# Kernel optimization log

Measured on AMD Instinct MI355X. Metric: run time of the kernel, lower is better.

Reference implementation:

```python
import jax, jax.numpy as jnp
import numpy as np

N = 50000      # nodes
E = 800000     # edges
H = 4          # heads (all layers)
D = 64         # per-head out dim (n_hidden == n_classes == 64)
IN = 256       # in_feats; also H*D so identity residual is valid
NEG_SLOPE = 0.2


def setup_inputs() -> dict:
    key = jax.random.key(0)
    ks = jax.random.split(key, 16)
    x = jax.random.normal(ks[0], (N, IN), dtype=jnp.float32)
    src = jax.random.randint(ks[1], (E,), 0, N, dtype=jnp.int32)
    dst = jax.random.randint(ks[2], (E,), 0, N, dtype=jnp.int32)
    inp = {"x": x, "src": src, "dst": dst}
    fan_ins = [IN, H * D, H * D]  # layer input widths
    for i, fin in enumerate(fan_ins):
        s = 1.0 / np.sqrt(fin)
        inp[f"W{i}"] = jax.random.normal(ks[3 + 4 * i], (fin, H * D), dtype=jnp.float32) * s
        inp[f"al{i}"] = jax.random.normal(ks[4 + 4 * i], (H, D), dtype=jnp.float32) * s
        inp[f"ar{i}"] = jax.random.normal(ks[5 + 4 * i], (H, D), dtype=jnp.float32) * s
        inp[f"b{i}"] = jnp.zeros((H * D,), dtype=jnp.float32)
    return inp


def _gat_layer(h, src, dst, W, al, ar, b, residual, activate):
    # project: [N, in] @ [in, H*D] -> [N, H, D]
    feat = (h @ W).reshape(-1, H, D)
    el = jnp.sum(feat * al, axis=-1)            # [N, H]
    er = jnp.sum(feat * ar, axis=-1)            # [N, H]
    e = jax.nn.leaky_relu(el[src] + er[dst], NEG_SLOPE)  # [E, H]
    # edge softmax per destination node (stable: subtract per-dst max)
    emax = jax.ops.segment_max(e, dst, num_segments=N)  # [N, H]
    e = jnp.exp(e - emax[dst])
    denom = jax.ops.segment_sum(e, dst, num_segments=N)  # [N, H]
    alpha = e / denom[dst]                               # [E, H]
    # message + scatter-aggregate: [E, H, D] summed into [N, H, D]
    out = jax.ops.segment_sum(alpha[:, :, None] * feat[src], dst, num_segments=N)
    if residual:
        out = out + h.reshape(-1, H, D)  # identity residual (in == H*D)
    out = out + b.reshape(1, H, D)
    if activate:
        out = jax.nn.elu(out)
    return out


def reference(x, src, dst, W0, al0, ar0, b0, W1, al1, ar1, b1, W2, al2, ar2, b2):
    h = _gat_layer(x, src, dst, W0, al0, ar0, b0, False, True).reshape(N, H * D)
    h = _gat_layer(h, src, dst, W1, al1, ar1, b1, True, True).reshape(N, H * D)
    h = _gat_layer(h, src, dst, W2, al2, ar2, b2, True, False).mean(axis=1)  # [N, D]
    return h
```

## Files before the change

### kernel.cpp

```cpp
#include <hip/hip_runtime.h>
#include <math.h>

#define N_NODES 50000
#define N_EDGES 800000
#define HD 256
#define NHEAD 4
#define DH 64

typedef short bf16x8 __attribute__((ext_vector_type(8)));
typedef float f32x4 __attribute__((ext_vector_type(4)));

__device__ __forceinline__ unsigned short f2bf(float f) {
    unsigned u = __float_as_uint(f);
    return (unsigned short)((u + 0x7fffu + ((u >> 16) & 1u)) >> 16);
}
__device__ __forceinline__ float bf2f(unsigned short h) {
    return __uint_as_float((unsigned)h << 16);
}

__global__ void packw_k(const float* __restrict__ W0, const float* __restrict__ W1,
                        const float* __restrict__ W2, unsigned short* __restrict__ Wp) {
    int blk = blockIdx.x;
    int L = blk >> 7, t = blk & 127;
    const float* W = L == 0 ? W0 : L == 1 ? W1 : W2;
    int nt = t >> 3, kt = t & 7;
    int lane = threadIdx.x;
    int col = nt * 16 + (lane & 15);
    int kb = kt * 32 + (lane >> 4) * 8;
    unsigned short v[8];
#pragma unroll
    for (int j = 0; j < 8; j++) v[j] = f2bf(W[(size_t)(kb + j) * 256 + col]);
    *(bf16x8*)(Wp + ((size_t)(L * 128 + t) * 64 + lane) * 8) = *(bf16x8*)v;
}

template <bool AFP32>
__global__ __launch_bounds__(256) void gemm_k(const void* __restrict__ Av,
                                              const unsigned short* __restrict__ Wp,
                                              const float* __restrict__ al,
                                              const float* __restrict__ ar,
                                              unsigned short* __restrict__ C,
                                              float* __restrict__ el,
                                              float* __restrict__ er, int M) {
    __shared__ unsigned short Asl[64 * 256];
    int tid = threadIdx.x, wv = tid >> 6, lane = tid & 63;
    int bm = blockIdx.x * 64;
    if (AFP32) {
        const float* A = (const float*)Av;
#pragma unroll
        for (int i = 0; i < 8; i++) {
            int chunk = i * 256 + tid;
            int r = chunk >> 5, kc = (chunk & 31) * 8;
            float4 f0, f1;
            if (bm + r < M) {
                const float* p = A + (size_t)(bm + r) * 256 + kc;
                f0 = *(const float4*)p;
                f1 = *(const float4*)(p + 4);
            } else {
                f0 = f1 = make_float4(0.f, 0.f, 0.f, 0.f);
            }
            unsigned short tmp[8] = {f2bf(f0.x), f2bf(f0.y), f2bf(f0.z), f2bf(f0.w),
                                     f2bf(f1.x), f2bf(f1.y), f2bf(f1.z), f2bf(f1.w)};
            int b = (r * 512 + kc * 2) ^ ((r & 7) << 4);
            *(bf16x8*)((char*)Asl + b) = *(bf16x8*)tmp;
        }
    } else {
        const unsigned short* A = (const unsigned short*)Av;
#pragma unroll
        for (int i = 0; i < 8; i++) {
            int chunk = i * 256 + tid;
            int r = chunk >> 5, c16 = chunk & 31;
            int grow = bm + r; if (grow >= M) grow = M - 1;
            bf16x8 v = *(const bf16x8*)(A + (size_t)grow * 256 + c16 * 8);
            int b = (r * 512 + c16 * 16) ^ ((r & 7) << 4);
            *(bf16x8*)((char*)Asl + b) = v;
        }
    }
    __syncthreads();
    f32x4 acc[4][4] = {};
    const unsigned short* wbase = Wp + (size_t)(wv * 4) * 8 * 64 * 8;
#pragma unroll
    for (int kk = 0; kk < 8; kk++) {
        bf16x8 a[4], b[4];
#pragma unroll
        for (int m = 0; m < 4; m++) {
            int r = m * 16 + (lane & 15);
            int kb = kk * 32 + (lane >> 4) * 8;
            int byt = (r * 512 + kb * 2) ^ ((r & 7) << 4);
            a[m] = *(const bf16x8*)((const char*)Asl + byt);
        }
#pragma unroll
        for (int n = 0; n < 4; n++)
            b[n] = *(const bf16x8*)(wbase + ((size_t)(n * 8 + kk) * 64 + lane) * 8);
#pragma unroll
        for (int m = 0; m < 4; m++)
#pragma unroll
            for (int n = 0; n < 4; n++)
                acc[m][n] = __builtin_amdgcn_mfma_f32_16x16x32_bf16(a[m], b[n],
                                                                    acc[m][n], 0, 0, 0);
    }
    int rr = lane >> 4, cc = lane & 15;
    float alv[4], arv[4];
#pragma unroll
    for (int n = 0; n < 4; n++) {
        alv[n] = al[wv * 64 + n * 16 + cc];
        arv[n] = ar[wv * 64 + n * 16 + cc];
    }
#pragma unroll
    for (int m = 0; m < 4; m++) {
#pragma unroll
        for (int r = 0; r < 4; r++) {
            int row = bm + m * 16 + rr * 4 + r;
            float ep = 0.f, rp = 0.f;
#pragma unroll
            for (int n = 0; n < 4; n++) {
                ep = fmaf(acc[m][n][r], alv[n], ep);
                rp = fmaf(acc[m][n][r], arv[n], rp);
            }
#pragma unroll
            for (int o = 1; o < 16; o <<= 1) {
                ep += __shfl_xor(ep, o);
                rp += __shfl_xor(rp, o);
            }
            if (row < M) {
                if (cc == 0) {
                    el[(size_t)row * NHEAD + wv] = ep;
                    er[(size_t)row * NHEAD + wv] = rp;
                }
#pragma unroll
                for (int n = 0; n < 4; n++)
                    C[(size_t)row * 256 + wv * 64 + n * 16 + cc] = f2bf(acc[m][n][r]);
            }
        }
    }
}

__global__ void hist_k(const int* __restrict__ dst, int* __restrict__ deg) {
    int e = blockIdx.x * 256 + threadIdx.x;
    if (e < N_EDGES) atomicAdd(&deg[dst[e]], 1);
}

__global__ __launch_bounds__(1024) void scan1_k(const int* __restrict__ deg,
                                                int* __restrict__ rowptr,
                                                int* __restrict__ bsum) {
    __shared__ int wsum[16];
    int tid = threadIdx.x, lane = tid & 63, wv = tid >> 6;
    int i = blockIdx.x * 1024 + tid;
    int v = (i < N_NODES) ? deg[i] : 0;
    int sc = v;
#pragma unroll
    for (int o = 1; o < 64; o <<= 1) {
        int t = __shfl_up(sc, o);
        if (lane >= o) sc += t;
    }
    if (lane == 63) wsum[wv] = sc;
    __syncthreads();
    if (wv == 0 && lane < 16) {
        int ws = wsum[lane];
#pragma unroll
        for (int o = 1; o < 16; o <<= 1) {
            int t = __shfl_up(ws, o);
            if (lane >= o) ws += t;
        }
        wsum[lane] = ws;
    }
    __syncthreads();
    int incl = sc + (wv > 0 ? wsum[wv - 1] : 0);
    if (i < N_NODES) rowptr[i + 1] = incl;
    if (tid == 1023) bsum[blockIdx.x] = incl;
}

__global__ __launch_bounds__(1024) void scan3_k(int* __restrict__ rowptr,
                                                const int* __restrict__ bsum,
                                                int* __restrict__ cursor, int nb) {
    __shared__ int boff_s;
    int tid = threadIdx.x;
    if (tid < 64) {
        int v = (tid < nb) ? bsum[tid] : 0;
        int sc = v;
#pragma unroll
        for (int o = 1; o < 64; o <<= 1) {
            int t = __shfl_up(sc, o);
            if ((tid & 63) >= o) sc += t;
        }
        if (tid == (int)blockIdx.x) boff_s = sc - v;
    }
    __syncthreads();
    int off = boff_s;
    int i = blockIdx.x * 1024 + tid;
    if (blockIdx.x == 0 && tid == 0) { rowptr[0] = 0; cursor[0] = 0; }
    if (i < N_NODES) {
        int v = rowptr[i + 1] + off;
        rowptr[i + 1] = v;
        if (i + 1 < N_NODES) cursor[i + 1] = v;
    }
}

__global__ void scatter_k(const int* __restrict__ src, const int* __restrict__ dst,
                          int* __restrict__ cursor, int* __restrict__ csr_src) {
    int e = blockIdx.x * 256 + threadIdx.x;
    if (e >= N_EDGES) return;
    int pos = atomicAdd(&cursor[dst[e]], 1);
    csr_src[pos] = src[e];
}

template <int MODE>
__global__ __launch_bounds__(256) void agg_k(const int* __restrict__ rowptr,
                                             const int* __restrict__ csr_src,
                                             const float* __restrict__ el,
                                             const float* __restrict__ er,
                                             const unsigned short* __restrict__ feat,
                                             const unsigned short* __restrict__ resid,
                                             const float* __restrict__ bias,
                                             float* __restrict__ out,
                                             unsigned short* __restrict__ hb) {
    __shared__ int   ws_s[4][64];
    __shared__ float ws_w[4][4][68];
    int wv = threadIdx.x >> 6, lane = threadIdx.x & 63;
    int node = blockIdx.x * 4 + wv;
    if (node >= N_NODES) return;
    int beg = rowptr[node], end = rowptr[node + 1];
    float4 er4 = *(const float4*)(er + (size_t)node * 4);
    float4 acc0 = make_float4(0.f, 0.f, 0.f, 0.f);
    float4 acc1 = make_float4(0.f, 0.f, 0.f, 0.f);
    float4 den = make_float4(0.f, 0.f, 0.f, 0.f);
    int h = lane >> 4;
    int l8 = lane * 8;
    const char* fb = (const char*)feat;
    for (int base = beg; base < end; base += 64) {
        int j = base + lane;
        int soff = 0;
        float4 w = make_float4(0.f, 0.f, 0.f, 0.f);
        if (j < end) {
            int s = csr_src[j];
            soff = s << 9;
            float4 l4 = *(const float4*)(el + (size_t)s * 4);
            float vx = l4.x + er4.x; vx = vx > 0.f ? vx : 0.2f * vx;
            float vy = l4.y + er4.y; vy = vy > 0.f ? vy : 0.2f * vy;
            float vz = l4.z + er4.z; vz = vz > 0.f ? vz : 0.2f * vz;
            float vw = l4.w + er4.w; vw = vw > 0.f ? vw : 0.2f * vw;
            w.x = expf(vx); w.y = expf(vy); w.z = expf(vz); w.w = expf(vw);
            den.x += w.x; den.y += w.y; den.z += w.z; den.w += w.w;
        }
        ws_s[wv][lane] = soff;
        ws_w[wv][0][lane] = w.x;
        ws_w[wv][1][lane] = w.y;
        ws_w[wv][2][lane] = w.z;
        ws_w[wv][3][lane] = w.w;
        __builtin_amdgcn_wave_barrier();
        int cnt = end - base; if (cnt > 64) cnt = 64;
        int cnt4 = (cnt + 3) & ~3;
        for (int k = 0; k < cnt4; k += 4) {
            int4   so = *(const int4*)&ws_s[wv][k];
            float4 w4 = *(const float4*)&ws_w[wv][h][k];
            ushort4 u0 = *(const ushort4*)(fb + (so.x + l8));
            ushort4 u1 = *(const ushort4*)(fb + (so.y + l8));
            ushort4 u2 = *(const ushort4*)(fb + (so.z + l8));
            ushort4 u3 = *(const ushort4*)(fb + (so.w + l8));
            acc0.x = fmaf(w4.x, bf2f(u0.x), acc0.x);
            acc0.y = fmaf(w4.x, bf2f(u0.y), acc0.y);
            acc0.z = fmaf(w4.x, bf2f(u0.z), acc0.z);
            acc0.w = fmaf(w4.x, bf2f(u0.w), acc0.w);
            acc1.x = fmaf(w4.y, bf2f(u1.x), acc1.x);
            acc1.y = fmaf(w4.y, bf2f(u1.y), acc1.y);
            acc1.z = fmaf(w4.y, bf2f(u1.z), acc1.z);
            acc1.w = fmaf(w4.y, bf2f(u1.w), acc1.w);
            acc0.x = fmaf(w4.z, bf2f(u2.x), acc0.x);
            acc0.y = fmaf(w4.z, bf2f(u2.y), acc0.y);
            acc0.z = fmaf(w4.z, bf2f(u2.z), acc0.z);
            acc0.w = fmaf(w4.z, bf2f(u2.w), acc0.w);
            acc1.x = fmaf(w4.w, bf2f(u3.x), acc1.x);
            acc1.y = fmaf(w4.w, bf2f(u3.y), acc1.y);
            acc1.z = fmaf(w4.w, bf2f(u3.z), acc1.z);
            acc1.w = fmaf(w4.w, bf2f(u3.w), acc1.w);
        }
        __builtin_amdgcn_wave_barrier();
    }
    float4 acc;
    acc.x = acc0.x + acc1.x; acc.y = acc0.y + acc1.y;
    acc.z = acc0.z + acc1.z; acc.w = acc0.w + acc1.w;
#pragma unroll
    for (int o = 1; o < 64; o <<= 1) {
        den.x += __shfl_xor(den.x, o);
        den.y += __shfl_xor(den.y, o);
        den.z += __shfl_xor(den.z, o);
        den.w += __shfl_xor(den.w, o);
    }
    float den_me = h == 0 ? den.x : h == 1 ? den.y : h == 2 ? den.z : den.w;
    float r = den_me > 0.f ? 1.f / den_me : 0.f;
    int col = lane * 4;
    float4 b4 = *(const float4*)(bias + col);
    float4 o4;
    o4.x = acc.x * r + b4.x;
    o4.y = acc.y * r + b4.y;
    o4.z = acc.z * r + b4.z;
    o4.w = acc.w * r + b4.w;
    if (MODE >= 1) {
        ushort4 r4 = *(const ushort4*)(resid + (size_t)node * HD + col);
        o4.x += bf2f(r4.x); o4.y += bf2f(r4.y);
        o4.z += bf2f(r4.z); o4.w += bf2f(r4.w);
    }
    if (MODE <= 1) {
        o4.x = o4.x > 0.f ? o4.x : expm1f(o4.x);
        o4.y = o4.y > 0.f ? o4.y : expm1f(o4.y);
        o4.z = o4.z > 0.f ? o4.z : expm1f(o4.z);
        o4.w = o4.w > 0.f ? o4.w : expm1f(o4.w);
        ushort4 hv;
        hv.x = f2bf(o4.x); hv.y = f2bf(o4.y); hv.z = f2bf(o4.z); hv.w = f2bf(o4.w);
        *(ushort4*)(hb + (size_t)node * HD + col) = hv;
    } else {
        o4.x += __shfl_xor(o4.x, 16); o4.x += __shfl_xor(o4.x, 32);
        o4.y += __shfl_xor(o4.y, 16); o4.y += __shfl_xor(o4.y, 32);
        o4.z += __shfl_xor(o4.z, 16); o4.z += __shfl_xor(o4.z, 32);
        o4.w += __shfl_xor(o4.w, 16); o4.w += __shfl_xor(o4.w, 32);
        if (lane < 16) {
            float4 ov = make_float4(o4.x * 0.25f, o4.y * 0.25f,
                                    o4.z * 0.25f, o4.w * 0.25f);
            *(float4*)(out + (size_t)node * DH + lane * 4) = ov;
        }
    }
}

extern "C" void kernel_launch(void* const* d_in, const int* in_sizes, int n_in,
                              void* d_out, int out_size, void* d_ws, size_t ws_size,
                              hipStream_t stream) {
    const float* x   = (const float*)d_in[0];
    const int*   src = (const int*)d_in[1];
    const int*   dst = (const int*)d_in[2];
    const float* W[3]  = {(const float*)d_in[3], (const float*)d_in[7],  (const float*)d_in[11]};
    const float* al[3] = {(const float*)d_in[4], (const float*)d_in[8],  (const float*)d_in[12]};
    const float* ar[3] = {(const float*)d_in[5], (const float*)d_in[9],  (const float*)d_in[13]};
    const float* bb[3] = {(const float*)d_in[6], (const float*)d_in[10], (const float*)d_in[14]};

    size_t big = (size_t)N_NODES * HD;
    unsigned short* featb = (unsigned short*)d_ws;
    unsigned short* hb1 = featb + big;
    unsigned short* hb2 = hb1 + big;
    float* el = (float*)(hb2 + big);
    float* er = el + (size_t)N_NODES * NHEAD;
    int* deg     = (int*)(er + (size_t)N_NODES * NHEAD);
    int* rowptr  = deg + 50048;
    int* cursor  = rowptr + 50048;
    int* csr_src = cursor + 50048;
    int* bsum    = csr_src + N_EDGES;
    unsigned short* Wp = (unsigned short*)(bsum + 64);

    const int NB = (N_NODES + 1023) / 1024;

    packw_k<<<384, 64, 0, stream>>>(W[0], W[1], W[2], Wp);
    hipMemsetAsync(deg, 0, (size_t)N_NODES * 4, stream);
    hist_k<<<N_EDGES / 256, 256, 0, stream>>>(dst, deg);
    scan1_k<<<NB, 1024, 0, stream>>>(deg, rowptr, bsum);
    scan3_k<<<NB, 1024, 0, stream>>>(rowptr, bsum, cursor, NB);
    scatter_k<<<N_EDGES / 256, 256, 0, stream>>>(src, dst, cursor, csr_src);

    int ggrid = (N_NODES + 63) / 64;
    int agrid = (N_NODES + 3) / 4;

    gemm_k<true><<<ggrid, 256, 0, stream>>>(x, Wp, al[0], ar[0], featb, el, er, N_NODES);
    agg_k<0><<<agrid, 256, 0, stream>>>(rowptr, csr_src, el, er, featb,
                                        nullptr, bb[0], nullptr, hb1);
    gemm_k<false><<<ggrid, 256, 0, stream>>>(hb1, Wp + (size_t)1 * 128 * 64 * 8,
                                             al[1], ar[1], featb, el, er, N_NODES);
    agg_k<1><<<agrid, 256, 0, stream>>>(rowptr, csr_src, el, er, featb,
                                        hb1, bb[1], nullptr, hb2);
    gemm_k<false><<<ggrid, 256, 0, stream>>>(hb2, Wp + (size_t)2 * 128 * 64 * 8,
                                             al[2], ar[2], featb, el, er, N_NODES);
    agg_k<2><<<agrid, 256, 0, stream>>>(rowptr, csr_src, el, er, featb,
                                        hb2, bb[2], (float*)d_out, nullptr);
}
```

Measured before the change: 358.6 us.

## Permute hidden feature layout for vector GEMM stores and use direct global-to-LDS loads

```diff
diff --git a/kernel.cpp b/kernel.cpp
--- a/kernel.cpp
+++ b/kernel.cpp
@@ -16,6 +16,9 @@
 }
 __device__ __forceinline__ float bf2f(unsigned short h) {
     return __uint_as_float((unsigned)h << 16);
+}
+__device__ __forceinline__ int origk(int k) {
+    return (k & ~63) | ((k & 3) * 16 + ((k >> 2) & 15));
 }
 
 __global__ void packw_k(const float* __restrict__ W0, const float* __restrict__ W1,
@@ -29,7 +32,11 @@
     int kb = kt * 32 + (lane >> 4) * 8;
     unsigned short v[8];
 #pragma unroll
-    for (int j = 0; j < 8; j++) v[j] = f2bf(W[(size_t)(kb + j) * 256 + col]);
+    for (int j = 0; j < 8; j++) {
+        int k = kb + j;
+        if (L > 0) k = origk(k);
+        v[j] = f2bf(W[(size_t)k * 256 + col]);
+    }
     *(bf16x8*)(Wp + ((size_t)(L * 128 + t) * 64 + lane) * 8) = *(bf16x8*)v;
 }
 
@@ -67,12 +74,15 @@
         const unsigned short* A = (const unsigned short*)Av;
 #pragma unroll
         for (int i = 0; i < 8; i++) {
-            int chunk = i * 256 + tid;
-            int r = chunk >> 5, c16 = chunk & 31;
-            int grow = bm + r; if (grow >= M) grow = M - 1;
-            bf16x8 v = *(const bf16x8*)(A + (size_t)grow * 256 + c16 * 8);
-            int b = (r * 512 + c16 * 16) ^ ((r & 7) << 4);
-            *(bf16x8*)((char*)Asl + b) = v;
+            int chunk = i * 256 + wv * 64 + lane;
+            int r = chunk >> 5;
+            int c16 = (chunk & 31) ^ (r & 7);
+            const unsigned short* src = A + (size_t)(bm + r) * 256 + c16 * 8;
+            __builtin_amdgcn_global_load_lds(
+                (const __attribute__((address_space(1))) unsigned int*)src,
+                (__attribute__((address_space(3))) unsigned int*)
+                    ((char*)Asl + (size_t)(i * 256 + wv * 64) * 16),
+                16, 0, 0);
         }
     }
     __syncthreads();
@@ -105,30 +115,72 @@
         alv[n] = al[wv * 64 + n * 16 + cc];
         arv[n] = ar[wv * 64 + n * 16 + cc];
     }
-#pragma unroll
-    for (int m = 0; m < 4; m++) {
+    float vl[16], vr[16];
+#pragma unroll
+    for (int m = 0; m < 4; m++)
 #pragma unroll
         for (int r = 0; r < 4; r++) {
-            int row = bm + m * 16 + rr * 4 + r;
             float ep = 0.f, rp = 0.f;
 #pragma unroll
             for (int n = 0; n < 4; n++) {
                 ep = fmaf(acc[m][n][r], alv[n], ep);
                 rp = fmaf(acc[m][n][r], arv[n], rp);
             }
-#pragma unroll
-            for (int o = 1; o < 16; o <<= 1) {
-                ep += __shfl_xor(ep, o);
-                rp += __shfl_xor(rp, o);
-            }
+            vl[m * 4 + r] = ep;
+            vr[m * 4 + r] = rp;
+        }
+    float l8[8], r8[8];
+#pragma unroll
+    for (int i = 0; i < 8; i++) {
+        float xs = (cc & 1) ? vl[2 * i] : vl[2 * i + 1];
+        float xk = (cc & 1) ? vl[2 * i + 1] : vl[2 * i];
+        l8[i] = xk + __shfl_xor(xs, 1);
+        float ys = (cc & 1) ? vr[2 * i] : vr[2 * i + 1];
+        float yk = (cc & 1) ? vr[2 * i + 1] : vr[2 * i];
+        r8[i] = yk + __shfl_xor(ys, 1);
+    }
+    float l4[4], r4[4];
+#pragma unroll
+    for (int i = 0; i < 4; i++) {
+        float xs = (cc & 2) ? l8[2 * i] : l8[2 * i + 1];
+        float xk = (cc & 2) ? l8[2 * i + 1] : l8[2 * i];
+        l4[i] = xk + __shfl_xor(xs, 2);
+        float ys = (cc & 2) ? r8[2 * i] : r8[2 * i + 1];
+        float yk = (cc & 2) ? r8[2 * i + 1] : r8[2 * i];
+        r4[i] = yk + __shfl_xor(ys, 2);
+    }
+    float l2[2], r2[2];
+#pragma unroll
+    for (int i = 0; i < 2; i++) {
+        float xs = (cc & 4) ? l4[2 * i] : l4[2 * i + 1];
+        float xk = (cc & 4) ? l4[2 * i + 1] : l4[2 * i];
+        l2[i] = xk + __shfl_xor(xs, 4);
+        float ys = (cc & 4) ? r4[2 * i] : r4[2 * i + 1];
+        float yk = (cc & 4) ? r4[2 * i + 1] : r4[2 * i];
+        r2[i] = yk + __shfl_xor(ys, 4);
+    }
+    {
+        float xs = (cc & 8) ? l2[0] : l2[1];
+        float xk = (cc & 8) ? l2[1] : l2[0];
+        float lv = xk + __shfl_xor(xs, 8);
+        float ys = (cc & 8) ? r2[0] : r2[1];
+        float yk = (cc & 8) ? r2[1] : r2[0];
+        float rv = yk + __shfl_xor(ys, 8);
+        int row_e = bm + (cc >> 2) * 16 + rr * 4 + (cc & 3);
+        if (row_e < M) {
+            el[(size_t)row_e * NHEAD + wv] = lv;
+            er[(size_t)row_e * NHEAD + wv] = rv;
+        }
+    }
+#pragma unroll
+    for (int m = 0; m < 4; m++) {
+#pragma unroll
+        for (int r = 0; r < 4; r++) {
+            int row = bm + m * 16 + rr * 4 + r;
             if (row < M) {
-                if (cc == 0) {
-                    el[(size_t)row * NHEAD + wv] = ep;
-                    er[(size_t)row * NHEAD + wv] = rp;
-                }
-#pragma unroll
-                for (int n = 0; n < 4; n++)
-                    C[(size_t)row * 256 + wv * 64 + n * 16 + cc] = f2bf(acc[m][n][r]);
+                unsigned short p4[4] = {f2bf(acc[m][0][r]), f2bf(acc[m][1][r]),
+                                        f2bf(acc[m][2][r]), f2bf(acc[m][3][r])};
+                *(ushort4*)(C + (size_t)row * 256 + wv * 64 + cc * 4) = *(ushort4*)p4;
             }
         }
     }
@@ -287,15 +339,19 @@
     }
     float den_me = h == 0 ? den.x : h == 1 ? den.y : h == 2 ? den.z : den.w;
     float r = den_me > 0.f ? 1.f / den_me : 0.f;
-    int col = lane * 4;
-    float4 b4 = *(const float4*)(bias + col);
+    int cc = lane & 15;
+    float4 b4;
+    b4.x = bias[h * 64 + 0 * 16 + cc];
+    b4.y = bias[h * 64 + 1 * 16 + cc];
+    b4.z = bias[h * 64 + 2 * 16 + cc];
+    b4.w = bias[h * 64 + 3 * 16 + cc];
     float4 o4;
     o4.x = acc.x * r + b4.x;
     o4.y = acc.y * r + b4.y;
     o4.z = acc.z * r + b4.z;
     o4.w = acc.w * r + b4.w;
     if (MODE >= 1) {
-        ushort4 r4 = *(const ushort4*)(resid + (size_t)node * HD + col);
+        ushort4 r4 = *(const ushort4*)(resid + (size_t)node * HD + lane * 4);
         o4.x += bf2f(r4.x); o4.y += bf2f(r4.y);
         o4.z += bf2f(r4.z); o4.w += bf2f(r4.w);
     }
@@ -306,16 +362,18 @@
         o4.w = o4.w > 0.f ? o4.w : expm1f(o4.w);
         ushort4 hv;
         hv.x = f2bf(o4.x); hv.y = f2bf(o4.y); hv.z = f2bf(o4.z); hv.w = f2bf(o4.w);
-        *(ushort4*)(hb + (size_t)node * HD + col) = hv;
+        *(ushort4*)(hb + (size_t)node * HD + lane * 4) = hv;
     } else {
         o4.x += __shfl_xor(o4.x, 16); o4.x += __shfl_xor(o4.x, 32);
         o4.y += __shfl_xor(o4.y, 16); o4.y += __shfl_xor(o4.y, 32);
         o4.z += __shfl_xor(o4.z, 16); o4.z += __shfl_xor(o4.z, 32);
         o4.w += __shfl_xor(o4.w, 16); o4.w += __shfl_xor(o4.w, 32);
         if (lane < 16) {
-            float4 ov = make_float4(o4.x * 0.25f, o4.y * 0.25f,
-                                    o4.z * 0.25f, o4.w * 0.25f);
-            *(float4*)(out + (size_t)node * DH + lane * 4) = ov;
+            float* po = out + (size_t)node * DH;
+            po[0 * 16 + lane] = o4.x * 0.25f;
+            po[1 * 16 + lane] = o4.y * 0.25f;
+            po[2 * 16 + lane] = o4.z * 0.25f;
+            po[3 * 16 + lane] = o4.w * 0.25f;
         }
     }
 }
```

Result: faster. 350.9 us (-2.1%).
